# Optimization experiments

Measured on AMD Instinct MI355X. Metric: run time of the kernel, lower is better.

Reference implementation:

```python
import jax, jax.numpy as jnp
import numpy as np

NUM_USER, NUM_ITEM, NUM_HIDDEN = 4096, 16384, 64
B, L = 1024, 50  # users in batch, items per user


def setup_inputs() -> dict:
    key = jax.random.key(0)
    k1, k2, k3, k4, k5 = jax.random.split(key, 5)
    return {
        "idx_user": jax.random.randint(k1, (B,), 0, NUM_USER),
        "item_sets": jax.random.randint(k2, (B, L), 0, NUM_ITEM),
        "rating_sets": jax.random.uniform(k3, (B, L), dtype=jnp.float32),
        "embed_user": 0.1 * jax.random.normal(k4, (NUM_USER, NUM_HIDDEN), dtype=jnp.float32),
        "embed_item": 0.1 * jax.random.normal(k5, (NUM_ITEM, NUM_HIDDEN), dtype=jnp.float32),
    }


def reference(idx_user, item_sets, rating_sets, embed_user, embed_item):
    # pred: [num_user, num_item] = U @ I^T
    pred = jnp.einsum("uh,ih->ui", embed_user, embed_item)
    # Vectorized scatter replacing the original nested Python loop:
    # rows broadcast to [B, L] so (row, col) pairs cover every rated entry.
    rows = idx_user[:, None]  # [B, 1] -> broadcasts against [B, L] items
    zeros = jnp.zeros((NUM_USER, NUM_ITEM), dtype=pred.dtype)
    mask = zeros.at[rows, item_sets].set(1.0)
    label = zeros.at[rows, item_sets].set(rating_sets)
    pred_mask = pred * mask
    sparsity = (NUM_USER * NUM_ITEM) / jnp.sum(mask)
    return pred_mask, label, sparsity
```

## Files before the change

### kernel.cpp

```cpp
#include <hip/hip_runtime.h>

#define NUM_USER   4096
#define NUM_ITEM   16384
#define NUM_HIDDEN 64
#define B_SZ       1024
#define L_SZ       50
#define KROWS      64
#define NBUCKET    1024

__global__ void build_rows_kernel(const int* __restrict__ idx_user,
                                  int* __restrict__ user_count,
                                  int* __restrict__ user_rows) {
    int b = blockIdx.x * blockDim.x + threadIdx.x;
    if (b < B_SZ) {
        int u = idx_user[b];
        int slot = atomicAdd(&user_count[u], 1);
        if (slot < KROWS) user_rows[u * KROWS + slot] = b;
    }
}

__global__ void scatter_kernel(const int* __restrict__ idx_user,
                               const int* __restrict__ item_sets,
                               const float* __restrict__ rating_sets,
                               const float* __restrict__ embed_user,
                               const float* __restrict__ embed_item,
                               float* __restrict__ pred_mask,
                               float* __restrict__ label,
                               const int* __restrict__ user_count,
                               const int* __restrict__ user_rows,
                               unsigned int* __restrict__ ucount) {
    const int p    = blockIdx.x;
    const int b    = p / L_SZ;
    const int l    = p - b * L_SZ;
    const int lane = threadIdx.x;

    const int u  = idx_user[b];
    const int it = item_sets[p];

    float a = embed_user[u * NUM_HIDDEN + lane];
    float c = embed_item[it * NUM_HIDDEN + lane];
    float v = a * c;
    #pragma unroll
    for (int m = 32; m >= 1; m >>= 1) v += __shfl_xor(v, m, 64);

    bool dup = false;
    if (lane > l && lane < L_SZ) dup = (item_sets[b * L_SZ + lane] == it);
    int cnt = user_count[u];
    if (cnt > KROWS) cnt = KROWS;
    for (int s = 0; s < cnt; ++s) {
        int b2 = user_rows[u * KROWS + s];
        if (b2 > b && lane < L_SZ) dup |= (item_sets[b2 * L_SZ + lane] == it);
    }
    unsigned long long anydup = __ballot(dup);

    if (lane == 0) {
        size_t cell = (size_t)u * NUM_ITEM + it;
        pred_mask[cell] = v;
        if (anydup == 0ull) {
            label[cell] = rating_sets[p];
            atomicAdd(&ucount[p & (NBUCKET - 1)], 1u);
        }
    }
}

__global__ void sparsity_kernel(const unsigned int* __restrict__ ucount,
                                float* __restrict__ out) {
    __shared__ unsigned int warp_sum[4];
    const int t = threadIdx.x;
    unsigned int s = 0;
    #pragma unroll
    for (int i = 0; i < NBUCKET / 256; ++i) s += ucount[t + i * 256];
    #pragma unroll
    for (int m = 32; m >= 1; m >>= 1) s += __shfl_xor(s, m, 64);
    if ((t & 63) == 0) warp_sum[t >> 6] = s;
    __syncthreads();
    if (t == 0) {
        unsigned int total = warp_sum[0] + warp_sum[1] + warp_sum[2] + warp_sum[3];
        out[0] = (float)((double)NUM_USER * (double)NUM_ITEM / (double)total);
    }
}

extern "C" void kernel_launch(void* const* d_in, const int* in_sizes, int n_in,
                              void* d_out, int out_size, void* d_ws, size_t ws_size,
                              hipStream_t stream) {
    const int*   idx_user    = (const int*)d_in[0];
    const int*   item_sets   = (const int*)d_in[1];
    const float* rating_sets = (const float*)d_in[2];
    const float* embed_user  = (const float*)d_in[3];
    const float* embed_item  = (const float*)d_in[4];

    float* pred_mask = (float*)d_out;
    float* label     = pred_mask + (size_t)NUM_USER * NUM_ITEM;
    float* sparsity  = label     + (size_t)NUM_USER * NUM_ITEM;

    int*          user_count = (int*)d_ws;
    int*          user_rows  = user_count + NUM_USER;
    unsigned int* ucount     = (unsigned int*)(user_rows + (size_t)NUM_USER * KROWS);

    hipMemsetAsync(d_out, 0, (size_t)out_size * sizeof(float), stream);
    hipMemsetAsync(d_ws, 0, (size_t)(NUM_USER * (KROWS + 1) + NBUCKET) * sizeof(int), stream);

    build_rows_kernel<<<(B_SZ + 255) / 256, 256, 0, stream>>>(idx_user, user_count, user_rows);
    scatter_kernel<<<B_SZ * L_SZ, 64, 0, stream>>>(idx_user, item_sets, rating_sets,
                                                   embed_user, embed_item,
                                                   pred_mask, label,
                                                   user_count, user_rows, ucount);
    sparsity_kernel<<<1, 256, 0, stream>>>(ucount, sparsity);
}
```

Before: 129.4 us.

## Fuse zero-fill and scatter into per-user segment gather kernel

Replaces the large output memset plus per-pair scatter kernel with one kernel that owns each user's 1024-item segment, computes any rated entries in it, and writes both outputs with float4 stores including zeros. Duplicate handling becomes last-write-wins by sequence index rather than a ballot across rows. This removes a separate full-buffer memset pass and the scattered single-float writes, but each block now scans all rated items of its user for every segment, which repeats index reads 16 times per user. The workspace memset shrinks because user_rows no longer needs clearing.

```diff
diff --git a/kernel.cpp b/kernel.cpp
--- a/kernel.cpp
+++ b/kernel.cpp
@@ -7,6 +7,8 @@
 #define L_SZ       50
 #define KROWS      64
 #define NBUCKET    1024
+#define SEG_ITEMS  1024
+#define SEGS_PER_USER (NUM_ITEM / SEG_ITEMS)
 
 __global__ void build_rows_kernel(const int* __restrict__ idx_user,
                                   int* __restrict__ user_count,
@@ -19,48 +21,63 @@
     }
 }
 
-__global__ void scatter_kernel(const int* __restrict__ idx_user,
-                               const int* __restrict__ item_sets,
-                               const float* __restrict__ rating_sets,
-                               const float* __restrict__ embed_user,
-                               const float* __restrict__ embed_item,
-                               float* __restrict__ pred_mask,
-                               float* __restrict__ label,
-                               const int* __restrict__ user_count,
-                               const int* __restrict__ user_rows,
-                               unsigned int* __restrict__ ucount) {
-    const int p    = blockIdx.x;
-    const int b    = p / L_SZ;
-    const int l    = p - b * L_SZ;
-    const int lane = threadIdx.x;
+__global__ void fused_fill_kernel(const int* __restrict__ item_sets,
+                                  const float* __restrict__ rating_sets,
+                                  const float* __restrict__ embed_user,
+                                  const float* __restrict__ embed_item,
+                                  const int* __restrict__ user_count,
+                                  const int* __restrict__ user_rows,
+                                  float* __restrict__ pred_mask,
+                                  float* __restrict__ label,
+                                  unsigned int* __restrict__ ucount) {
+    const int unit = blockIdx.x;
+    const int u    = unit >> 4;
+    const int seg  = unit & (SEGS_PER_USER - 1);
+    const int t    = threadIdx.x;
+    const int lane = t & 63;
+    const int jt   = seg * SEG_ITEMS + t * 4;
 
-    const int u  = idx_user[b];
-    const int it = item_sets[p];
+    float4 pv = {0.f, 0.f, 0.f, 0.f};
+    float4 lv = {0.f, 0.f, 0.f, 0.f};
+    int bs0 = -1, bs1 = -1, bs2 = -1, bs3 = -1;
 
-    float a = embed_user[u * NUM_HIDDEN + lane];
-    float c = embed_item[it * NUM_HIDDEN + lane];
-    float v = a * c;
-    #pragma unroll
-    for (int m = 32; m >= 1; m >>= 1) v += __shfl_xor(v, m, 64);
+    int r = user_count[u];
+    if (r > KROWS) r = KROWS;
 
-    bool dup = false;
-    if (lane > l && lane < L_SZ) dup = (item_sets[b * L_SZ + lane] == it);
-    int cnt = user_count[u];
-    if (cnt > KROWS) cnt = KROWS;
-    for (int s = 0; s < cnt; ++s) {
-        int b2 = user_rows[u * KROWS + s];
-        if (b2 > b && lane < L_SZ) dup |= (item_sets[b2 * L_SZ + lane] == it);
+    if (r > 0) {
+        const int   wj0 = seg * SEG_ITEMS + (t >> 6) * 256;
+        const float eu  = embed_user[u * NUM_HIDDEN + lane];
+        for (int s = 0; s < r; ++s) {
+            const int b       = user_rows[u * KROWS + s];
+            const int rowbase = b * L_SZ;
+            for (int l = 0; l < L_SZ; ++l) {
+                const int it = item_sets[rowbase + l];
+                if ((unsigned)(it - wj0) < 256u) {
+                    float v = eu * embed_item[it * NUM_HIDDEN + lane];
+                    #pragma unroll
+                    for (int m = 32; m >= 1; m >>= 1) v += __shfl_xor(v, m, 64);
+                    const int rel = it - jt;
+                    if ((unsigned)rel < 4u) {
+                        const int seq = rowbase + l;
+                        const float rating = rating_sets[rowbase + l];
+                        if (rel == 0)      { pv.x = v; if (seq > bs0) { bs0 = seq; lv.x = rating; } }
+                        else if (rel == 1) { pv.y = v; if (seq > bs1) { bs1 = seq; lv.y = rating; } }
+                        else if (rel == 2) { pv.z = v; if (seq > bs2) { bs2 = seq; lv.z = rating; } }
+                        else               { pv.w = v; if (seq > bs3) { bs3 = seq; lv.w = rating; } }
+                    }
+                }
+            }
+        }
+        unsigned int n = (bs0 >= 0) + (bs1 >= 0) + (bs2 >= 0) + (bs3 >= 0);
+        #pragma unroll
+        for (int m = 32; m >= 1; m >>= 1) n += __shfl_xor(n, m, 64);
+        if (lane == 0 && n > 0)
+            atomicAdd(&ucount[unit & (NBUCKET - 1)], n);
     }
-    unsigned long long anydup = __ballot(dup);
 
-    if (lane == 0) {
-        size_t cell = (size_t)u * NUM_ITEM + it;
-        pred_mask[cell] = v;
-        if (anydup == 0ull) {
-            label[cell] = rating_sets[p];
-            atomicAdd(&ucount[p & (NBUCKET - 1)], 1u);
-        }
-    }
+    const size_t cell = (size_t)u * NUM_ITEM + jt;
+    *(float4*)(pred_mask + cell) = pv;
+    *(float4*)(label     + cell) = lv;
 }
 
 __global__ void sparsity_kernel(const unsigned int* __restrict__ ucount,
@@ -94,16 +111,14 @@
     float* sparsity  = label     + (size_t)NUM_USER * NUM_ITEM;
 
     int*          user_count = (int*)d_ws;
-    int*          user_rows  = user_count + NUM_USER;
-    unsigned int* ucount     = (unsigned int*)(user_rows + (size_t)NUM_USER * KROWS);
+    unsigned int* ucount     = (unsigned int*)(user_count + NUM_USER);
+    int*          user_rows  = (int*)(ucount + NBUCKET);
 
-    hipMemsetAsync(d_out, 0, (size_t)out_size * sizeof(float), stream);
-    hipMemsetAsync(d_ws, 0, (size_t)(NUM_USER * (KROWS + 1) + NBUCKET) * sizeof(int), stream);
+    hipMemsetAsync(d_ws, 0, (size_t)(NUM_USER + NBUCKET) * sizeof(int), stream);
 
     build_rows_kernel<<<(B_SZ + 255) / 256, 256, 0, stream>>>(idx_user, user_count, user_rows);
-    scatter_kernel<<<B_SZ * L_SZ, 64, 0, stream>>>(idx_user, item_sets, rating_sets,
-                                                   embed_user, embed_item,
-                                                   pred_mask, label,
-                                                   user_count, user_rows, ucount);
+    fused_fill_kernel<<<NUM_USER * SEGS_PER_USER, 256, 0, stream>>>(
+        item_sets, rating_sets, embed_user, embed_item,
+        user_count, user_rows, pred_mask, label, ucount);
     sparsity_kernel<<<1, 256, 0, stream>>>(ucount, sparsity);
 }
```

Measured after the change: 150.2 us. 1.16x slower.

## Bucket pairs by row segment and fuse zero-fill with scatter writes

Applied to the files above, without the earlier changes.

Replaces the full-output memset and per-pair scatter with a two-phase scheme. Pairs are first binned into 1024-item row segments. A fill kernel then writes each segment of pred_mask and label with float4 stores, injecting the winning (last-written) pair values and counting unique cells. This removes the separate memset pass over the large output and the costly per-pair duplicate search, at the cost of workspace buckets, atomics, and a per-thread linear scan of each bucket.

```diff
diff --git a/kernel.cpp b/kernel.cpp
--- a/kernel.cpp
+++ b/kernel.cpp
@@ -5,62 +5,88 @@
 #define NUM_HIDDEN 64
 #define B_SZ       1024
 #define L_SZ       50
-#define KROWS      64
+#define NPAIR      (B_SZ * L_SZ)
+#define SEG_ITEMS  1024
+#define NSEG       (NUM_USER * (NUM_ITEM / SEG_ITEMS))
+#define CAP        64
 #define NBUCKET    1024
 
-__global__ void build_rows_kernel(const int* __restrict__ idx_user,
-                                  int* __restrict__ user_count,
-                                  int* __restrict__ user_rows) {
-    int b = blockIdx.x * blockDim.x + threadIdx.x;
-    if (b < B_SZ) {
-        int u = idx_user[b];
-        int slot = atomicAdd(&user_count[u], 1);
-        if (slot < KROWS) user_rows[u * KROWS + slot] = b;
+__global__ void pair_kernel(const int* __restrict__ idx_user,
+                            const int* __restrict__ item_sets,
+                            const float* __restrict__ rating_sets,
+                            const float* __restrict__ embed_user,
+                            const float* __restrict__ embed_item,
+                            unsigned int* __restrict__ seg_count,
+                            unsigned int* __restrict__ seg_key,
+                            float* __restrict__ seg_val,
+                            float* __restrict__ seg_rat) {
+    const int p    = blockIdx.x * 4 + (threadIdx.x >> 6);
+    const int lane = threadIdx.x & 63;
+    if (p >= NPAIR) return;
+    const int b  = p / L_SZ;
+    const int u  = idx_user[b];
+    const int it = item_sets[p];
+
+    float v = embed_user[u * NUM_HIDDEN + lane] * embed_item[it * NUM_HIDDEN + lane];
+    #pragma unroll
+    for (int m = 32; m >= 1; m >>= 1) v += __shfl_xor(v, m, 64);
+
+    if (lane == 0) {
+        const int seg = u * (NUM_ITEM / SEG_ITEMS) + (it >> 10);
+        unsigned int slot = atomicAdd(&seg_count[seg], 1u);
+        if (slot < CAP) {
+            const int base = seg * CAP + (int)slot;
+            seg_key[base] = ((unsigned int)p << 10) | (unsigned int)(it & (SEG_ITEMS - 1));
+            seg_val[base] = v;
+            seg_rat[base] = rating_sets[p];
+        }
     }
 }
 
-__global__ void scatter_kernel(const int* __restrict__ idx_user,
-                               const int* __restrict__ item_sets,
-                               const float* __restrict__ rating_sets,
-                               const float* __restrict__ embed_user,
-                               const float* __restrict__ embed_item,
-                               float* __restrict__ pred_mask,
-                               float* __restrict__ label,
-                               const int* __restrict__ user_count,
-                               const int* __restrict__ user_rows,
-                               unsigned int* __restrict__ ucount) {
-    const int p    = blockIdx.x;
-    const int b    = p / L_SZ;
-    const int l    = p - b * L_SZ;
-    const int lane = threadIdx.x;
+__global__ void fill_inject_kernel(const unsigned int* __restrict__ seg_count,
+                                   const unsigned int* __restrict__ seg_key,
+                                   const float* __restrict__ seg_val,
+                                   const float* __restrict__ seg_rat,
+                                   float* __restrict__ pred_mask,
+                                   float* __restrict__ label,
+                                   unsigned int* __restrict__ ucount) {
+    const int seg = blockIdx.x;
+    const int t   = threadIdx.x;
+    const size_t cell = (size_t)seg * SEG_ITEMS + t * 4;
 
-    const int u  = idx_user[b];
-    const int it = item_sets[p];
+    float4 pv = {0.f, 0.f, 0.f, 0.f};
+    float4 lv = {0.f, 0.f, 0.f, 0.f};
 
-    float a = embed_user[u * NUM_HIDDEN + lane];
-    float c = embed_item[it * NUM_HIDDEN + lane];
-    float v = a * c;
-    #pragma unroll
-    for (int m = 32; m >= 1; m >>= 1) v += __shfl_xor(v, m, 64);
+    unsigned int k = seg_count[seg];
+    if (k > CAP) k = CAP;
 
-    bool dup = false;
-    if (lane > l && lane < L_SZ) dup = (item_sets[b * L_SZ + lane] == it);
-    int cnt = user_count[u];
-    if (cnt > KROWS) cnt = KROWS;
-    for (int s = 0; s < cnt; ++s) {
-        int b2 = user_rows[u * KROWS + s];
-        if (b2 > b && lane < L_SZ) dup |= (item_sets[b2 * L_SZ + lane] == it);
+    if (k > 0) {
+        int bk0 = -1, bk1 = -1, bk2 = -1, bk3 = -1;
+        int bi0 = 0,  bi1 = 0,  bi2 = 0,  bi3 = 0;
+        const int base = seg * CAP;
+        const int j0   = t * 4;
+        for (int i = 0; i < (int)k; ++i) {
+            const int key  = (int)seg_key[base + i];
+            const int rel  = (key & (SEG_ITEMS - 1)) - j0;
+            bool m0 = (rel == 0) && (key > bk0); bk0 = m0 ? key : bk0; bi0 = m0 ? i : bi0;
+            bool m1 = (rel == 1) && (key > bk1); bk1 = m1 ? key : bk1; bi1 = m1 ? i : bi1;
+            bool m2 = (rel == 2) && (key > bk2); bk2 = m2 ? key : bk2; bi2 = m2 ? i : bi2;
+            bool m3 = (rel == 3) && (key > bk3); bk3 = m3 ? key : bk3; bi3 = m3 ? i : bi3;
+        }
+        if (bk0 >= 0) { pv.x = seg_val[base + bi0]; lv.x = seg_rat[base + bi0]; }
+        if (bk1 >= 0) { pv.y = seg_val[base + bi1]; lv.y = seg_rat[base + bi1]; }
+        if (bk2 >= 0) { pv.z = seg_val[base + bi2]; lv.z = seg_rat[base + bi2]; }
+        if (bk3 >= 0) { pv.w = seg_val[base + bi3]; lv.w = seg_rat[base + bi3]; }
+
+        unsigned int n = (bk0 >= 0) + (bk1 >= 0) + (bk2 >= 0) + (bk3 >= 0);
+        #pragma unroll
+        for (int m = 32; m >= 1; m >>= 1) n += __shfl_xor(n, m, 64);
+        if ((t & 63) == 0 && n > 0)
+            atomicAdd(&ucount[seg & (NBUCKET - 1)], n);
     }
-    unsigned long long anydup = __ballot(dup);
 
-    if (lane == 0) {
-        size_t cell = (size_t)u * NUM_ITEM + it;
-        pred_mask[cell] = v;
-        if (anydup == 0ull) {
-            label[cell] = rating_sets[p];
-            atomicAdd(&ucount[p & (NBUCKET - 1)], 1u);
-        }
-    }
+    *(float4*)(pred_mask + cell) = pv;
+    *(float4*)(label     + cell) = lv;
 }
 
 __global__ void sparsity_kernel(const unsigned int* __restrict__ ucount,
@@ -93,17 +119,18 @@
     float* label     = pred_mask + (size_t)NUM_USER * NUM_ITEM;
     float* sparsity  = label     + (size_t)NUM_USER * NUM_ITEM;
 
-    int*          user_count = (int*)d_ws;
-    int*          user_rows  = user_count + NUM_USER;
-    unsigned int* ucount     = (unsigned int*)(user_rows + (size_t)NUM_USER * KROWS);
+    unsigned int* seg_count = (unsigned int*)d_ws;
+    unsigned int* ucount    = seg_count + NSEG;
+    unsigned int* seg_key   = ucount + NBUCKET;
+    float*        seg_val   = (float*)(seg_key + (size_t)NSEG * CAP);
+    float*        seg_rat   = seg_val + (size_t)NSEG * CAP;
 
-    hipMemsetAsync(d_out, 0, (size_t)out_size * sizeof(float), stream);
-    hipMemsetAsync(d_ws, 0, (size_t)(NUM_USER * (KROWS + 1) + NBUCKET) * sizeof(int), stream);
+    hipMemsetAsync(d_ws, 0, (size_t)(NSEG + NBUCKET) * sizeof(int), stream);
 
-    build_rows_kernel<<<(B_SZ + 255) / 256, 256, 0, stream>>>(idx_user, user_count, user_rows);
-    scatter_kernel<<<B_SZ * L_SZ, 64, 0, stream>>>(idx_user, item_sets, rating_sets,
-                                                   embed_user, embed_item,
-                                                   pred_mask, label,
-                                                   user_count, user_rows, ucount);
+    pair_kernel<<<NPAIR / 4, 256, 0, stream>>>(idx_user, item_sets, rating_sets,
+                                               embed_user, embed_item,
+                                               seg_count, seg_key, seg_val, seg_rat);
+    fill_inject_kernel<<<NSEG, 256, 0, stream>>>(seg_count, seg_key, seg_val, seg_rat,
+                                                 pred_mask, label, ucount);
     sparsity_kernel<<<1, 256, 0, stream>>>(ucount, sparsity);
 }
```

Measured after the change: 142.5 us. +10.1%, slower.
